# Optimization experiments

Hardware: AMD Instinct MI355X
Metric: run time of the kernel (lower is better)

The kernel has to match this reference:

```python
import jax, jax.numpy as jnp
import numpy as np

D_MODEL = 1024
N_HEADS = 16
HEAD_DIM = D_MODEL // N_HEADS


def setup_inputs() -> dict:
    key = jax.random.key(0)
    ks = jax.random.split(key, 9)
    B, S = 4, 2048
    x = jax.random.normal(ks[0], (B, S, D_MODEL), dtype=jnp.float32)
    # causal mask, broadcastable to (B, H, S, S); mask==0 -> -inf
    mask = jnp.tril(jnp.ones((S, S), dtype=jnp.int32))[None, None, :, :]
    s = 1.0 / np.sqrt(D_MODEL)
    wq = jax.random.normal(ks[1], (D_MODEL, D_MODEL), dtype=jnp.float32) * s
    wk = jax.random.normal(ks[2], (D_MODEL, D_MODEL), dtype=jnp.float32) * s
    wv = jax.random.normal(ks[3], (D_MODEL, D_MODEL), dtype=jnp.float32) * s
    wo = jax.random.normal(ks[4], (D_MODEL, D_MODEL), dtype=jnp.float32) * s
    bq = jnp.zeros((D_MODEL,), jnp.float32)
    bk = jnp.zeros((D_MODEL,), jnp.float32)
    bv = jnp.zeros((D_MODEL,), jnp.float32)
    bo = jnp.zeros((D_MODEL,), jnp.float32)
    return {"x": x, "mask": mask, "wq": wq, "bq": bq, "wk": wk, "bk": bk,
            "wv": wv, "bv": bv, "wo": wo, "bo": bo}


def reference(x, mask, wq, bq, wk, bk, wv, bv, wo, bo):
    B, S, D = x.shape
    H, Hd = N_HEADS, HEAD_DIM
    # torch nn.Linear: y = x @ W^T + b
    q = (jnp.einsum('bsd,ed->bse', x, wq) + bq).reshape(B, S, H, Hd).transpose(0, 2, 1, 3)
    k = (jnp.einsum('bsd,ed->bse', x, wk) + bk).reshape(B, S, H, Hd).transpose(0, 2, 1, 3)
    v = (jnp.einsum('bsd,ed->bse', x, wv) + bv).reshape(B, S, H, Hd).transpose(0, 2, 1, 3)
    scores = jnp.einsum('bhqd,bhkd->bhqk', q, k) / jnp.sqrt(jnp.float32(Hd))
    scores = jnp.where(mask == 0, -jnp.inf, scores)
    attn = jax.nn.softmax(scores, axis=-1)
    out = jnp.einsum('bhqk,bhkd->bhqd', attn, v)  # (B,H,S,Hd)
    out = out.transpose(0, 2, 1, 3).reshape(B, S, D)
    return jnp.einsum('bsd,ed->bse', out, wo) + bo
```

## Files before the change

kernel.cpp:

```cpp
#include <hip/hip_runtime.h>
#include <hip/hip_bf16.h>
#include <math.h>

using bf16x8 = __attribute__((ext_vector_type(8))) __bf16;
using bf16x4 = __attribute__((ext_vector_type(4))) __bf16;
using f32x4  = __attribute__((ext_vector_type(4))) float;
using f32x16 = __attribute__((ext_vector_type(16))) float;
using u32x4  = __attribute__((ext_vector_type(4))) unsigned;

static constexpr int S_ = 2048;
static constexpr float SCALE_L2E = 0.125f * 1.44269504088896340736f;

__device__ __forceinline__ void gload16(const void* g, void* lds) {
    __builtin_amdgcn_global_load_lds((const __attribute__((address_space(1))) void*)g,
                                     (__attribute__((address_space(3))) void*)lds, 16, 0, 0);
}

__device__ __forceinline__ unsigned pk2(float a, float b) {
    unsigned short lo = __builtin_bit_cast(unsigned short, (__bf16)a);
    unsigned short hi = __builtin_bit_cast(unsigned short, (__bf16)b);
    return (unsigned)lo | ((unsigned)hi << 16);
}

__device__ __forceinline__ float max3f(float a, float b, float c) {
    return fmaxf(fmaxf(a, b), c);
}

__global__ void cast_f32_bf16(const float* __restrict__ src, __bf16* __restrict__ dst, int n4) {
    int i = blockIdx.x * blockDim.x + threadIdx.x;
    if (i < n4) {
        float4 v = reinterpret_cast<const float4*>(src)[i];
        bf16x4 o = { (__bf16)v.x, (__bf16)v.y, (__bf16)v.z, (__bf16)v.w };
        reinterpret_cast<bf16x4*>(dst)[i] = o;
    }
}

template <int EPI>
__global__ __launch_bounds__(256) void gemm_bt(
    const __bf16* __restrict__ A, const __bf16* __restrict__ Bt,
    const float* __restrict__ b0, const float* __restrict__ b1, const float* __restrict__ b2,
    __bf16* __restrict__ Qo, __bf16* __restrict__ Ko, __bf16* __restrict__ Vo,
    float* __restrict__ Fo, int K) {
    __shared__ __align__(16) __bf16 LDS_[3][2][4096];
    const int t = threadIdx.x, l = t & 63, w = t >> 6;
    const int m0 = blockIdx.y * 128, n0 = blockIdx.x * 128;
    const int wm = (w >> 1) * 64, wn = (w & 1) * 64;
    f32x4 acc[4][4] = {};

    const int row0 = t >> 2, cw0 = t & 3;
    const int gc = cw0 ^ ((row0 >> 1) & 3);
    const __bf16* Ag0 = A + (size_t)(m0 + row0) * K + gc * 8;
    const __bf16* Ag1 = A + (size_t)(m0 + row0 + 64) * K + gc * 8;
    const __bf16* Bg0 = Bt + (size_t)(n0 + row0) * K + gc * 8;
    const __bf16* Bg1 = Bt + (size_t)(n0 + row0 + 64) * K + gc * 8;
    const int wo512 = w * 512;

#define STAGE(buf, k0)                                          \
    do {                                                        \
        gload16(Ag0 + (k0), &LDS_[buf][0][wo512]);              \
        gload16(Ag1 + (k0), &LDS_[buf][0][2048 + wo512]);       \
        gload16(Bg0 + (k0), &LDS_[buf][1][wo512]);              \
        gload16(Bg1 + (k0), &LDS_[buf][1][2048 + wo512]);       \
    } while (0)

    const int nk = K >> 5;
    STAGE(0, 0);
    STAGE(1, 32);
    int rb = 0, sb = 2;
    const int sc = (l >> 4) ^ ((l >> 1) & 3);
    for (int ki = 0; ki < nk; ++ki) {
        if (ki + 2 < nk) {
            STAGE(sb, (ki + 2) << 5);
            asm volatile("s_waitcnt vmcnt(8)" ::: "memory");
        } else if (ki + 1 < nk) {
            asm volatile("s_waitcnt vmcnt(4)" ::: "memory");
        } else {
            asm volatile("s_waitcnt vmcnt(0)" ::: "memory");
        }
        __builtin_amdgcn_s_barrier();
        const char* rdA = (const char*)&LDS_[rb][0][0];
        const char* rdB = (const char*)&LDS_[rb][1][0];
        bf16x8 af[4], bf[4];
#pragma unroll
        for (int i = 0; i < 4; ++i)
            af[i] = *reinterpret_cast<const bf16x8*>(rdA + (wm + i * 16 + (l & 15)) * 64 + sc * 16);
#pragma unroll
        for (int j = 0; j < 4; ++j)
            bf[j] = *reinterpret_cast<const bf16x8*>(rdB + (wn + j * 16 + (l & 15)) * 64 + sc * 16);
#pragma unroll
        for (int i = 0; i < 4; ++i)
#pragma unroll
            for (int j = 0; j < 4; ++j)
                acc[i][j] = __builtin_amdgcn_mfma_f32_16x16x32_bf16(af[i], bf[j], acc[i][j], 0, 0, 0);
        __builtin_amdgcn_s_barrier();
        rb = (rb == 2) ? 0 : rb + 1;
        sb = (sb == 2) ? 0 : sb + 1;
    }
#undef STAGE

    if (EPI == 0) {
        const int cls = n0 >> 10;
        if (cls < 2) {
            const float* bias = (cls == 0) ? b0 : b1;
#pragma unroll
            for (int j = 0; j < 4; ++j) {
                const int e = n0 + wn + j * 16 + (l & 15);
                const int eh = e & 1023;
                const int h = eh >> 6, hd = eh & 63;
                const float bv = bias[eh];
#pragma unroll
                for (int i = 0; i < 4; ++i)
#pragma unroll
                    for (int r = 0; r < 4; ++r) {
                        const int m = m0 + wm + i * 16 + ((l >> 4) << 2) + r;
                        const int b = m >> 11, s = m & 2047;
                        float v = acc[i][j][r] + bv;
                        if (cls == 0) v *= SCALE_L2E;
                        __bf16* dst = (cls == 0) ? Qo : Ko;
                        dst[((size_t)(b * 16 + h) * 2048 + s) * 64 + hd] = (__bf16)v;
                    }
            }
        } else {
            char* Tr = (char*)&LDS_[0][0][0];
#pragma unroll
            for (int j = 0; j < 4; ++j) {
                const int el = wn + j * 16 + (l & 15);
                const float bv = b2[(n0 & 1023) + el];
#pragma unroll
                for (int i = 0; i < 4; ++i) {
                    const int m4 = wm + i * 16 + ((l >> 4) << 2);
                    const int pos0 = (m4 & 112) | ((m4 & 4) << 1) | ((m4 & 8) >> 1);
                    bf16x4 pkv = { (__bf16)(acc[i][j][0] + bv), (__bf16)(acc[i][j][1] + bv),
                                   (__bf16)(acc[i][j][2] + bv), (__bf16)(acc[i][j][3] + bv) };
                    const int byt = el * 256 + ((pos0 * 2) ^ ((el & 7) << 4));
                    *reinterpret_cast<bf16x4*>(Tr + byt) = pkv;
                }
            }
            __syncthreads();
            const int b = m0 >> 11, sblk = m0 & 2047;
#pragma unroll
            for (int rr = 0; rr < 8; ++rr) {
                const int er = w * 32 + rr * 4 + (l >> 4);
                const int c = l & 15;
                const int slot = c ^ (er & 7);
                bf16x8 vv = *reinterpret_cast<const bf16x8*>(Tr + er * 256 + slot * 16);
                const int eg = (n0 & 1023) + er;
                const int h = eg >> 6, hd = eg & 63;
                char* dst = (char*)(Vo + ((size_t)(b * 16 + h) * 64 + hd) * 2048 + sblk) + c * 16;
                *reinterpret_cast<bf16x8*>(dst) = vv;
            }
        }
    } else {
#pragma unroll
        for (int j = 0; j < 4; ++j) {
            const int e = n0 + wn + j * 16 + (l & 15);
            const float bv = b0[e];
#pragma unroll
            for (int i = 0; i < 4; ++i)
#pragma unroll
                for (int r = 0; r < 4; ++r) {
                    const int m = m0 + wm + i * 16 + ((l >> 4) << 2) + r;
                    Fo[(size_t)m * 1024 + e] = acc[i][j][r] + bv;
                }
        }
    }
}

__global__ __launch_bounds__(512, 4) void attn_fwd(
    const __bf16* __restrict__ Qb, const __bf16* __restrict__ Kb,
    const __bf16* __restrict__ VTb, __bf16* __restrict__ Ob) {
    __shared__ __align__(16) __bf16 Ks[2][64 * 64];
    __shared__ __align__(16) __bf16 Vs[2][64 * 64];
    const int t = threadIdx.x, l = t & 63, w = t >> 6;
    const int id = blockIdx.x;
    const int bh = (id & 7) * 8 + ((id >> 3) & 7);
    const int g = id >> 6;
    const int xp = (g < 4) ? g : 11 - g;
    const int b = bh >> 4, hh = bh & 15;
    const int hl = l >> 5, l31 = l & 31;

    const __bf16* Qg = Qb + (size_t)bh * S_ * 64;
    const __bf16* Kg = Kb + (size_t)bh * S_ * 64;
    const __bf16* Vg = VTb + (size_t)bh * 64 * S_;

    const int qt = (w >> 2) ? xp : (15 - xp);
    const int sw = w & 3;
    const int qs = qt * 128 + sw * 32;
    const int qg = qs + l31;

    const int l3 = l >> 3, gc8 = ((l & 7) ^ l3) * 8;
    const __bf16* Ksrc = Kg + (size_t)(8 * w + l3) * 64 + gc8;
    const __bf16* Vsrc = Vg + (size_t)(8 * w + l3) * S_ + gc8;
    __bf16* Kd0 = &Ks[0][w * 512]; __bf16* Kd1 = &Ks[1][w * 512];
    __bf16* Vd0 = &Vs[0][w * 512]; __bf16* Vd1 = &Vs[1][w * 512];

    bf16x8 qf[4];
#pragma unroll
    for (int c = 0; c < 4; ++c)
        qf[c] = *reinterpret_cast<const bf16x8*>(Qg + (size_t)qg * 64 + c * 16 + hl * 8);

    f32x16 o0 = {}, o1 = {};
    float m_r = -INFINITY, l_r = 0.f;

    const int ktmax_blk = 2 * (15 - xp) + 1;
    gload16(Ksrc, Kd0);
    gload16(Vsrc, Vd0);
    int cur = 0;
    for (int kt = 0; kt <= ktmax_blk; ++kt) {
        if (kt < ktmax_blk) {
            const size_t ko = (size_t)(kt + 1) * 4096;
            gload16(Ksrc + ko, (cur == 0) ? Kd1 : Kd0);
            gload16(Vsrc + (kt + 1) * 64, (cur == 0) ? Vd1 : Vd0);
            asm volatile("s_waitcnt vmcnt(2)" ::: "memory");
        } else {
            asm volatile("s_waitcnt vmcnt(0)" ::: "memory");
        }
        __builtin_amdgcn_s_barrier();
        const char* kb = (cur == 0) ? (const char*)Ks[0] : (const char*)Ks[1];
        const char* vb = (cur == 0) ? (const char*)Vs[0] : (const char*)Vs[1];
        if (kt * 64 <= qs + 31) {
            const int xs = (l & 7) << 4;
            f32x16 s0 = {}, s1 = {};
            __builtin_amdgcn_s_setprio(1);
#pragma unroll
            for (int c = 0; c < 4; ++c) {
                bf16x8 kf0 = *reinterpret_cast<const bf16x8*>(kb + l31 * 128 + ((c * 32 + hl * 16) ^ xs));
                s0 = __builtin_amdgcn_mfma_f32_32x32x16_bf16(kf0, qf[c], s0, 0, 0, 0);
            }
#pragma unroll
            for (int c = 0; c < 4; ++c) {
                bf16x8 kf1 = *reinterpret_cast<const bf16x8*>(kb + (32 + l31) * 128 + ((c * 32 + hl * 16) ^ xs));
                s1 = __builtin_amdgcn_mfma_f32_32x32x16_bf16(kf1, qf[c], s1, 0, 0, 0);
            }
            __builtin_amdgcn_s_setprio(0);
            float p0[16], p1[16];
            const int ktb = kt * 64;
            const bool bnd = (ktb + 63) > qs;
            if (bnd) {
#pragma unroll
                for (int r = 0; r < 16; ++r) {
                    const int kvr = ktb + (r & 3) + 8 * (r >> 2) + 4 * hl;
                    p0[r] = (kvr > qg) ? -INFINITY : s0[r];
                    p1[r] = (kvr + 32 > qg) ? -INFINITY : s1[r];
                }
            } else {
#pragma unroll
                for (int r = 0; r < 16; ++r) { p0[r] = s0[r]; p1[r] = s1[r]; }
            }
            float mx[16];
#pragma unroll
            for (int r = 0; r < 16; ++r) mx[r] = fmaxf(p0[r], p1[r]);
            float u0 = max3f(mx[0], mx[1], mx[2]);
            float u1 = max3f(mx[3], mx[4], mx[5]);
            float u2 = max3f(mx[6], mx[7], mx[8]);
            float u3 = max3f(mx[9], mx[10], mx[11]);
            float u4 = max3f(mx[12], mx[13], mx[14]);
            float mt = fmaxf(max3f(u0, u1, u2), max3f(u3, u4, mx[15]));
            mt = fmaxf(mt, __shfl_xor(mt, 32));
            if (!__all(mt - m_r <= 8.0f)) {
                const float mn = fmaxf(m_r, mt);
                const float al = exp2f(m_r - mn);
                m_r = mn;
                l_r *= al;
#pragma unroll
                for (int r = 0; r < 16; ++r) { o0[r] *= al; o1[r] *= al; }
            }
            float sm[16];
#pragma unroll
            for (int r = 0; r < 16; ++r) {
                p0[r] = exp2f(p0[r] - m_r);
                p1[r] = exp2f(p1[r] - m_r);
                sm[r] = p0[r] + p1[r];
            }
#pragma unroll
            for (int s2 = 8; s2 > 0; s2 >>= 1)
#pragma unroll
                for (int r = 0; r < 8; ++r) if (r < s2) sm[r] += sm[r + s2];
            l_r += sm[0] + __shfl_xor(sm[0], 32);
            u32x4 w0 = { pk2(p0[0], p0[1]), pk2(p0[2], p0[3]), pk2(p0[4], p0[5]), pk2(p0[6], p0[7]) };
            u32x4 w1 = { pk2(p0[8], p0[9]), pk2(p0[10], p0[11]), pk2(p0[12], p0[13]), pk2(p0[14], p0[15]) };
            u32x4 w2 = { pk2(p1[0], p1[1]), pk2(p1[2], p1[3]), pk2(p1[4], p1[5]), pk2(p1[6], p1[7]) };
            u32x4 w3 = { pk2(p1[8], p1[9]), pk2(p1[10], p1[11]), pk2(p1[12], p1[13]), pk2(p1[14], p1[15]) };
            bf16x8 pf0 = __builtin_bit_cast(bf16x8, w0);
            bf16x8 pf1 = __builtin_bit_cast(bf16x8, w1);
            bf16x8 pf2 = __builtin_bit_cast(bf16x8, w2);
            bf16x8 pf3 = __builtin_bit_cast(bf16x8, w3);
            __builtin_amdgcn_s_setprio(1);
#pragma unroll
            for (int a = 0; a < 2; ++a) {
                const int rb2 = (a * 32 + l31) * 128;
                bf16x8 vf0 = *reinterpret_cast<const bf16x8*>(vb + rb2 + ((0 * 32 + hl * 16) ^ xs));
                bf16x8 vf1 = *reinterpret_cast<const bf16x8*>(vb + rb2 + ((1 * 32 + hl * 16) ^ xs));
                bf16x8 vf2 = *reinterpret_cast<const bf16x8*>(vb + rb2 + ((2 * 32 + hl * 16) ^ xs));
                bf16x8 vf3 = *reinterpret_cast<const bf16x8*>(vb + rb2 + ((3 * 32 + hl * 16) ^ xs));
                if (a == 0) {
                    o0 = __builtin_amdgcn_mfma_f32_32x32x16_bf16(vf0, pf0, o0, 0, 0, 0);
                    o0 = __builtin_amdgcn_mfma_f32_32x32x16_bf16(vf1, pf1, o0, 0, 0, 0);
                    o0 = __builtin_amdgcn_mfma_f32_32x32x16_bf16(vf2, pf2, o0, 0, 0, 0);
                    o0 = __builtin_amdgcn_mfma_f32_32x32x16_bf16(vf3, pf3, o0, 0, 0, 0);
                } else {
                    o1 = __builtin_amdgcn_mfma_f32_32x32x16_bf16(vf0, pf0, o1, 0, 0, 0);
                    o1 = __builtin_amdgcn_mfma_f32_32x32x16_bf16(vf1, pf1, o1, 0, 0, 0);
                    o1 = __builtin_amdgcn_mfma_f32_32x32x16_bf16(vf2, pf2, o1, 0, 0, 0);
                    o1 = __builtin_amdgcn_mfma_f32_32x32x16_bf16(vf3, pf3, o1, 0, 0, 0);
                }
            }
            __builtin_amdgcn_s_setprio(0);
        }
        __builtin_amdgcn_s_barrier();
        cur ^= 1;
    }
    const float inv = 1.0f / l_r;
    __bf16* ob = Ob + (size_t)(b * 2048 + qg) * 1024 + hh * 64;
#pragma unroll
    for (int gq = 0; gq < 4; ++gq) {
        bf16x4 v0 = { (__bf16)(o0[4 * gq + 0] * inv), (__bf16)(o0[4 * gq + 1] * inv),
                      (__bf16)(o0[4 * gq + 2] * inv), (__bf16)(o0[4 * gq + 3] * inv) };
        bf16x4 v1 = { (__bf16)(o1[4 * gq + 0] * inv), (__bf16)(o1[4 * gq + 1] * inv),
                      (__bf16)(o1[4 * gq + 2] * inv), (__bf16)(o1[4 * gq + 3] * inv) };
        *reinterpret_cast<bf16x4*>(ob + 8 * gq + 4 * hl) = v0;
        *reinterpret_cast<bf16x4*>(ob + 32 + 8 * gq + 4 * hl) = v1;
    }
}

extern "C" void kernel_launch(void* const* d_in, const int* in_sizes, int n_in,
                              void* d_out, int out_size, void* d_ws, size_t ws_size,
                              hipStream_t stream) {
    const float* x  = (const float*)d_in[0];
    const float* wq = (const float*)d_in[2];
    const float* bq = (const float*)d_in[3];
    const float* wk = (const float*)d_in[4];
    const float* bk = (const float*)d_in[5];
    const float* wv = (const float*)d_in[6];
    const float* bv = (const float*)d_in[7];
    const float* wo = (const float*)d_in[8];
    const float* bo = (const float*)d_in[9];
    float* out = (float*)d_out;

    char* ws = (char*)d_ws;
    __bf16* xb   = (__bf16*)(ws);
    __bf16* wqkv = (__bf16*)(ws + 16777216);
    __bf16* wob  = (__bf16*)(ws + 23068672);
    __bf16* Qb   = (__bf16*)(ws + 25165824);
    __bf16* Kb   = (__bf16*)(ws + 41943040);
    __bf16* VTb  = (__bf16*)(ws + 58720256);
    __bf16* Ob   = (__bf16*)(ws + 75497472);

    cast_f32_bf16<<<8192, 256, 0, stream>>>(x, xb, 2097152);
    cast_f32_bf16<<<1024, 256, 0, stream>>>(wq, wqkv, 262144);
    cast_f32_bf16<<<1024, 256, 0, stream>>>(wk, wqkv + 1048576, 262144);
    cast_f32_bf16<<<1024, 256, 0, stream>>>(wv, wqkv + 2097152, 262144);
    cast_f32_bf16<<<1024, 256, 0, stream>>>(wo, wob, 262144);

    gemm_bt<0><<<dim3(24, 64), 256, 0, stream>>>(xb, wqkv, bq, bk, bv, Qb, Kb, VTb, nullptr, 1024);
    attn_fwd<<<512, 512, 0, stream>>>(Qb, Kb, VTb, Ob);
    gemm_bt<1><<<dim3(8, 64), 256, 0, stream>>>(Ob, wob, bo, nullptr, nullptr, nullptr, nullptr, nullptr, out, 1024);
}
```

Measured before the change: 185.0 us.

## Shrink attention blocks to two waves with 32-row KV tiles and paired phases

The attention kernel now runs as 1024 blocks of 128 threads instead of 512 blocks of 512 threads. Each block covers 64 query rows and processes two mirrored query tiles in sequence, which balances the causal workload within a block. KV tiles are cut from 64 to 32 keys with a new LDS swizzle for V. The goal is less barrier coupling across waves and more resident blocks per CU. In exchange there are twice as many loop iterations and barriers per query tile, and less reuse of each staged K/V tile, since only two waves share it.

```diff
diff --git a/kernel.cpp b/kernel.cpp
--- a/kernel.cpp
+++ b/kernel.cpp
@@ -166,16 +166,16 @@
     }
 }
 
-__global__ __launch_bounds__(512, 4) void attn_fwd(
+__global__ __launch_bounds__(128, 4) void attn_fwd(
     const __bf16* __restrict__ Qb, const __bf16* __restrict__ Kb,
     const __bf16* __restrict__ VTb, __bf16* __restrict__ Ob) {
-    __shared__ __align__(16) __bf16 Ks[2][64 * 64];
-    __shared__ __align__(16) __bf16 Vs[2][64 * 64];
+    __shared__ __align__(16) __bf16 Ks[2][32 * 64];
+    __shared__ __align__(16) __bf16 Vs[2][64 * 32];
     const int t = threadIdx.x, l = t & 63, w = t >> 6;
     const int id = blockIdx.x;
     const int bh = (id & 7) * 8 + ((id >> 3) & 7);
-    const int g = id >> 6;
-    const int xp = (g < 4) ? g : 11 - g;
+    const int pp = (id >> 6) & 7;
+    const int hf = id >> 9;
     const int b = bh >> 4, hh = bh & 15;
     const int hl = l >> 5, l31 = l & 31;
 
@@ -183,144 +183,137 @@
     const __bf16* Kg = Kb + (size_t)bh * S_ * 64;
     const __bf16* Vg = VTb + (size_t)bh * 64 * S_;
 
-    const int qt = (w >> 2) ? xp : (15 - xp);
-    const int sw = w & 3;
-    const int qs = qt * 128 + sw * 32;
-    const int qg = qs + l31;
-
-    const int l3 = l >> 3, gc8 = ((l & 7) ^ l3) * 8;
-    const __bf16* Ksrc = Kg + (size_t)(8 * w + l3) * 64 + gc8;
-    const __bf16* Vsrc = Vg + (size_t)(8 * w + l3) * S_ + gc8;
-    __bf16* Kd0 = &Ks[0][w * 512]; __bf16* Kd1 = &Ks[1][w * 512];
-    __bf16* Vd0 = &Vs[0][w * 512]; __bf16* Vd1 = &Vs[1][w * 512];
-
-    bf16x8 qf[4];
-#pragma unroll
-    for (int c = 0; c < 4; ++c)
-        qf[c] = *reinterpret_cast<const bf16x8*>(Qg + (size_t)qg * 64 + c * 16 + hl * 8);
-
-    f32x16 o0 = {}, o1 = {};
-    float m_r = -INFINITY, l_r = 0.f;
-
-    const int ktmax_blk = 2 * (15 - xp) + 1;
-    gload16(Ksrc, Kd0);
-    gload16(Vsrc, Vd0);
-    int cur = 0;
-    for (int kt = 0; kt <= ktmax_blk; ++kt) {
-        if (kt < ktmax_blk) {
-            const size_t ko = (size_t)(kt + 1) * 4096;
-            gload16(Ksrc + ko, (cur == 0) ? Kd1 : Kd0);
-            gload16(Vsrc + (kt + 1) * 64, (cur == 0) ? Vd1 : Vd0);
-            asm volatile("s_waitcnt vmcnt(2)" ::: "memory");
-        } else {
-            asm volatile("s_waitcnt vmcnt(0)" ::: "memory");
-        }
-        __builtin_amdgcn_s_barrier();
-        const char* kb = (cur == 0) ? (const char*)Ks[0] : (const char*)Ks[1];
-        const char* vb = (cur == 0) ? (const char*)Vs[0] : (const char*)Vs[1];
-        if (kt * 64 <= qs + 31) {
-            const int xs = (l & 7) << 4;
-            f32x16 s0 = {}, s1 = {};
-            __builtin_amdgcn_s_setprio(1);
-#pragma unroll
-            for (int c = 0; c < 4; ++c) {
-                bf16x8 kf0 = *reinterpret_cast<const bf16x8*>(kb + l31 * 128 + ((c * 32 + hl * 16) ^ xs));
-                s0 = __builtin_amdgcn_mfma_f32_32x32x16_bf16(kf0, qf[c], s0, 0, 0, 0);
-            }
-#pragma unroll
-            for (int c = 0; c < 4; ++c) {
-                bf16x8 kf1 = *reinterpret_cast<const bf16x8*>(kb + (32 + l31) * 128 + ((c * 32 + hl * 16) ^ xs));
-                s1 = __builtin_amdgcn_mfma_f32_32x32x16_bf16(kf1, qf[c], s1, 0, 0, 0);
-            }
-            __builtin_amdgcn_s_setprio(0);
-            float p0[16], p1[16];
-            const int ktb = kt * 64;
-            const bool bnd = (ktb + 63) > qs;
-            if (bnd) {
-#pragma unroll
-                for (int r = 0; r < 16; ++r) {
-                    const int kvr = ktb + (r & 3) + 8 * (r >> 2) + 4 * hl;
-                    p0[r] = (kvr > qg) ? -INFINITY : s0[r];
-                    p1[r] = (kvr + 32 > qg) ? -INFINITY : s1[r];
-                }
+    const int l3 = l >> 3;
+    const int kc8 = ((l & 7) ^ l3) * 8;
+    const __bf16* Ksrc0 = Kg + (size_t)(16 * w + l3) * 64 + kc8;
+    const __bf16* Ksrc1 = Kg + (size_t)(16 * w + 8 + l3) * 64 + kc8;
+    const int l2 = l >> 2;
+    const int vc8 = ((l & 3) ^ (l2 & 3)) * 8;
+    const __bf16* Vsrc0 = Vg + (size_t)(32 * w + l2) * S_ + vc8;
+    const __bf16* Vsrc1 = Vg + (size_t)(32 * w + 16 + l2) * S_ + vc8;
+    __bf16* Kd0 = &Ks[0][w * 1024]; __bf16* Kd1 = &Ks[1][w * 1024];
+    __bf16* Vd0 = &Vs[0][w * 1024]; __bf16* Vd1 = &Vs[1][w * 1024];
+
+#define STAGEKV(cc, kt)                                                   \
+    do {                                                                  \
+        gload16(Ksrc0 + (size_t)(kt) * 2048, (cc) ? Kd1 : Kd0);           \
+        gload16(Ksrc1 + (size_t)(kt) * 2048, ((cc) ? Kd1 : Kd0) + 512);   \
+        gload16(Vsrc0 + (kt) * 32, (cc) ? Vd1 : Vd0);                     \
+        gload16(Vsrc1 + (kt) * 32, ((cc) ? Vd1 : Vd0) + 512);             \
+    } while (0)
+
+#pragma unroll 1
+    for (int ph = 0; ph < 2; ++ph) {
+        const int qt = ph ? pp : (15 - pp);
+        const int qs = qt * 128 + hf * 64 + w * 32;
+        const int qg = qs + l31;
+
+        bf16x8 qf[4];
+#pragma unroll
+        for (int c = 0; c < 4; ++c)
+            qf[c] = *reinterpret_cast<const bf16x8*>(Qg + (size_t)qg * 64 + c * 16 + hl * 8);
+
+        f32x16 o0 = {}, o1 = {};
+        float m_r = -INFINITY, l_r = 0.f;
+
+        const int nkt = 4 * qt + 4;
+        STAGEKV(0, 0);
+        int cur = 0;
+        for (int kt = 0; kt < nkt; ++kt) {
+            if (kt + 1 < nkt) {
+                STAGEKV(cur ^ 1, kt + 1);
+                asm volatile("s_waitcnt vmcnt(4)" ::: "memory");
             } else {
-#pragma unroll
-                for (int r = 0; r < 16; ++r) { p0[r] = s0[r]; p1[r] = s1[r]; }
-            }
-            float mx[16];
-#pragma unroll
-            for (int r = 0; r < 16; ++r) mx[r] = fmaxf(p0[r], p1[r]);
-            float u0 = max3f(mx[0], mx[1], mx[2]);
-            float u1 = max3f(mx[3], mx[4], mx[5]);
-            float u2 = max3f(mx[6], mx[7], mx[8]);
-            float u3 = max3f(mx[9], mx[10], mx[11]);
-            float u4 = max3f(mx[12], mx[13], mx[14]);
-            float mt = fmaxf(max3f(u0, u1, u2), max3f(u3, u4, mx[15]));
-            mt = fmaxf(mt, __shfl_xor(mt, 32));
-            if (!__all(mt - m_r <= 8.0f)) {
-                const float mn = fmaxf(m_r, mt);
-                const float al = exp2f(m_r - mn);
-                m_r = mn;
-                l_r *= al;
-#pragma unroll
-                for (int r = 0; r < 16; ++r) { o0[r] *= al; o1[r] *= al; }
-            }
-            float sm[16];
-#pragma unroll
-            for (int r = 0; r < 16; ++r) {
-                p0[r] = exp2f(p0[r] - m_r);
-                p1[r] = exp2f(p1[r] - m_r);
-                sm[r] = p0[r] + p1[r];
-            }
-#pragma unroll
-            for (int s2 = 8; s2 > 0; s2 >>= 1)
-#pragma unroll
-                for (int r = 0; r < 8; ++r) if (r < s2) sm[r] += sm[r + s2];
-            l_r += sm[0] + __shfl_xor(sm[0], 32);
-            u32x4 w0 = { pk2(p0[0], p0[1]), pk2(p0[2], p0[3]), pk2(p0[4], p0[5]), pk2(p0[6], p0[7]) };
-            u32x4 w1 = { pk2(p0[8], p0[9]), pk2(p0[10], p0[11]), pk2(p0[12], p0[13]), pk2(p0[14], p0[15]) };
-            u32x4 w2 = { pk2(p1[0], p1[1]), pk2(p1[2], p1[3]), pk2(p1[4], p1[5]), pk2(p1[6], p1[7]) };
-            u32x4 w3 = { pk2(p1[8], p1[9]), pk2(p1[10], p1[11]), pk2(p1[12], p1[13]), pk2(p1[14], p1[15]) };
-            bf16x8 pf0 = __builtin_bit_cast(bf16x8, w0);
-            bf16x8 pf1 = __builtin_bit_cast(bf16x8, w1);
-            bf16x8 pf2 = __builtin_bit_cast(bf16x8, w2);
-            bf16x8 pf3 = __builtin_bit_cast(bf16x8, w3);
-            __builtin_amdgcn_s_setprio(1);
-#pragma unroll
-            for (int a = 0; a < 2; ++a) {
-                const int rb2 = (a * 32 + l31) * 128;
-                bf16x8 vf0 = *reinterpret_cast<const bf16x8*>(vb + rb2 + ((0 * 32 + hl * 16) ^ xs));
-                bf16x8 vf1 = *reinterpret_cast<const bf16x8*>(vb + rb2 + ((1 * 32 + hl * 16) ^ xs));
-                bf16x8 vf2 = *reinterpret_cast<const bf16x8*>(vb + rb2 + ((2 * 32 + hl * 16) ^ xs));
-                bf16x8 vf3 = *reinterpret_cast<const bf16x8*>(vb + rb2 + ((3 * 32 + hl * 16) ^ xs));
-                if (a == 0) {
-                    o0 = __builtin_amdgcn_mfma_f32_32x32x16_bf16(vf0, pf0, o0, 0, 0, 0);
-                    o0 = __builtin_amdgcn_mfma_f32_32x32x16_bf16(vf1, pf1, o0, 0, 0, 0);
-                    o0 = __builtin_amdgcn_mfma_f32_32x32x16_bf16(vf2, pf2, o0, 0, 0, 0);
-                    o0 = __builtin_amdgcn_mfma_f32_32x32x16_bf16(vf3, pf3, o0, 0, 0, 0);
+                asm volatile("s_waitcnt vmcnt(0)" ::: "memory");
+            }
+            __builtin_amdgcn_s_barrier();
+            const char* kb = (const char*)(cur ? Ks[1] : Ks[0]);
+            const char* vb = (const char*)(cur ? Vs[1] : Vs[0]);
+            const int ktb = kt * 32;
+            if (ktb <= qs + 31) {
+                const int xs = (l31 & 7) << 4;
+                f32x16 s0 = {};
+                __builtin_amdgcn_s_setprio(1);
+#pragma unroll
+                for (int c = 0; c < 4; ++c) {
+                    bf16x8 kf = *reinterpret_cast<const bf16x8*>(kb + l31 * 128 + ((c * 32 + hl * 16) ^ xs));
+                    s0 = __builtin_amdgcn_mfma_f32_32x32x16_bf16(kf, qf[c], s0, 0, 0, 0);
+                }
+                __builtin_amdgcn_s_setprio(0);
+                float pr[16];
+                const bool bnd = (ktb + 31) > qs;
+                if (bnd) {
+#pragma unroll
+                    for (int r = 0; r < 16; ++r) {
+                        const int kvr = ktb + (r & 3) + 8 * (r >> 2) + 4 * hl;
+                        pr[r] = (kvr > qg) ? -INFINITY : s0[r];
+                    }
                 } else {
-                    o1 = __builtin_amdgcn_mfma_f32_32x32x16_bf16(vf0, pf0, o1, 0, 0, 0);
-                    o1 = __builtin_amdgcn_mfma_f32_32x32x16_bf16(vf1, pf1, o1, 0, 0, 0);
-                    o1 = __builtin_amdgcn_mfma_f32_32x32x16_bf16(vf2, pf2, o1, 0, 0, 0);
-                    o1 = __builtin_amdgcn_mfma_f32_32x32x16_bf16(vf3, pf3, o1, 0, 0, 0);
-                }
-            }
-            __builtin_amdgcn_s_setprio(0);
-        }
-        __builtin_amdgcn_s_barrier();
-        cur ^= 1;
+#pragma unroll
+                    for (int r = 0; r < 16; ++r) pr[r] = s0[r];
+                }
+                float u0 = max3f(pr[0], pr[1], pr[2]);
+                float u1 = max3f(pr[3], pr[4], pr[5]);
+                float u2 = max3f(pr[6], pr[7], pr[8]);
+                float u3 = max3f(pr[9], pr[10], pr[11]);
+                float u4 = max3f(pr[12], pr[13], pr[14]);
+                float mt = fmaxf(max3f(u0, u1, u2), max3f(u3, u4, pr[15]));
+                mt = fmaxf(mt, __shfl_xor(mt, 32));
+                if (!__all(mt - m_r <= 8.0f)) {
+                    const float mn = fmaxf(m_r, mt);
+                    const float al = exp2f(m_r - mn);
+                    m_r = mn;
+                    l_r *= al;
+#pragma unroll
+                    for (int r = 0; r < 16; ++r) { o0[r] *= al; o1[r] *= al; }
+                }
+                float sm[8];
+#pragma unroll
+                for (int r = 0; r < 16; ++r) pr[r] = exp2f(pr[r] - m_r);
+#pragma unroll
+                for (int r = 0; r < 8; ++r) sm[r] = pr[r] + pr[r + 8];
+#pragma unroll
+                for (int s2 = 4; s2 > 0; s2 >>= 1)
+#pragma unroll
+                    for (int r = 0; r < 4; ++r) if (r < s2) sm[r] += sm[r + s2];
+                l_r += sm[0] + __shfl_xor(sm[0], 32);
+                u32x4 w0 = { pk2(pr[0], pr[1]), pk2(pr[2], pr[3]), pk2(pr[4], pr[5]), pk2(pr[6], pr[7]) };
+                u32x4 w1 = { pk2(pr[8], pr[9]), pk2(pr[10], pr[11]), pk2(pr[12], pr[13]), pk2(pr[14], pr[15]) };
+                bf16x8 pf0 = __builtin_bit_cast(bf16x8, w0);
+                bf16x8 pf1 = __builtin_bit_cast(bf16x8, w1);
+                __builtin_amdgcn_s_setprio(1);
+                const int xv = l31 & 3;
+#pragma unroll
+                for (int a = 0; a < 2; ++a) {
+                    const int rb2 = (a * 32 + l31) * 64;
+                    bf16x8 vf0 = *reinterpret_cast<const bf16x8*>(vb + rb2 + (((0 + hl) ^ xv) << 4));
+                    bf16x8 vf1 = *reinterpret_cast<const bf16x8*>(vb + rb2 + (((2 + hl) ^ xv) << 4));
+                    if (a == 0) {
+                        o0 = __builtin_amdgcn_mfma_f32_32x32x16_bf16(vf0, pf0, o0, 0, 0, 0);
+                        o0 = __builtin_amdgcn_mfma_f32_32x32x16_bf16(vf1, pf1, o0, 0, 0, 0);
+                    } else {
+                        o1 = __builtin_amdgcn_mfma_f32_32x32x16_bf16(vf0, pf0, o1, 0, 0, 0);
+                        o1 = __builtin_amdgcn_mfma_f32_32x32x16_bf16(vf1, pf1, o1, 0, 0, 0);
+                    }
+                }
+                __builtin_amdgcn_s_setprio(0);
+            }
+            __builtin_amdgcn_s_barrier();
+            cur ^= 1;
+        }
+        const float inv = 1.0f / l_r;
+        __bf16* ob = Ob + (size_t)(b * 2048 + qg) * 1024 + hh * 64;
+#pragma unroll
+        for (int gq = 0; gq < 4; ++gq) {
+            bf16x4 v0 = { (__bf16)(o0[4 * gq + 0] * inv), (__bf16)(o0[4 * gq + 1] * inv),
+                          (__bf16)(o0[4 * gq + 2] * inv), (__bf16)(o0[4 * gq + 3] * inv) };
+            bf16x4 v1 = { (__bf16)(o1[4 * gq + 0] * inv), (__bf16)(o1[4 * gq + 1] * inv),
+                          (__bf16)(o1[4 * gq + 2] * inv), (__bf16)(o1[4 * gq + 3] * inv) };
+            *reinterpret_cast<bf16x4*>(ob + 8 * gq + 4 * hl) = v0;
+            *reinterpret_cast<bf16x4*>(ob + 32 + 8 * gq + 4 * hl) = v1;
+        }
     }
-    const float inv = 1.0f / l_r;
-    __bf16* ob = Ob + (size_t)(b * 2048 + qg) * 1024 + hh * 64;
-#pragma unroll
-    for (int gq = 0; gq < 4; ++gq) {
-        bf16x4 v0 = { (__bf16)(o0[4 * gq + 0] * inv), (__bf16)(o0[4 * gq + 1] * inv),
-                      (__bf16)(o0[4 * gq + 2] * inv), (__bf16)(o0[4 * gq + 3] * inv) };
-        bf16x4 v1 = { (__bf16)(o1[4 * gq + 0] * inv), (__bf16)(o1[4 * gq + 1] * inv),
-                      (__bf16)(o1[4 * gq + 2] * inv), (__bf16)(o1[4 * gq + 3] * inv) };
-        *reinterpret_cast<bf16x4*>(ob + 8 * gq + 4 * hl) = v0;
-        *reinterpret_cast<bf16x4*>(ob + 32 + 8 * gq + 4 * hl) = v1;
-    }
+#undef STAGEKV
 }
 
 extern "C" void kernel_launch(void* const* d_in, const int* in_sizes, int n_in,
@@ -353,6 +346,6 @@
     cast_f32_bf16<<<1024, 256, 0, stream>>>(wo, wob, 262144);
 
     gemm_bt<0><<<dim3(24, 64), 256, 0, stream>>>(xb, wqkv, bq, bk, bv, Qb, Kb, VTb, nullptr, 1024);
-    attn_fwd<<<512, 512, 0, stream>>>(Qb, Kb, VTb, Ob);
+    attn_fwd<<<1024, 128, 0, stream>>>(Qb, Kb, VTb, Ob);
     gemm_bt<1><<<dim3(8, 64), 256, 0, stream>>>(Ob, wob, bo, nullptr, nullptr, nullptr, nullptr, nullptr, out, 1024);
 }
```

Result: slower. 202.0 us (+9.2%).

## Split attention into one q-tile per 4-warp block with interleaved causal ordering

Applied to the files above, without the earlier changes.

Each attention block now processes a single 128-row query tile with 4 warps instead of pairing a heavy and a light tile in 8 warps. This removes the idle warps of the light tile that previously waited through the heavy tile's extra K/V iterations and barriers. The block index ordering interleaves long and short tiles to keep the GPU load balanced, and K/V staging is redistributed so each thread issues four async loads per stage. The risk is a longer tail from the heaviest blocks and less K/V reuse per load across warps.

```diff
diff --git a/kernel.cpp b/kernel.cpp
--- a/kernel.cpp
+++ b/kernel.cpp
@@ -166,16 +166,16 @@
     }
 }
 
-__global__ __launch_bounds__(512, 4) void attn_fwd(
+__global__ __launch_bounds__(256, 4) void attn_fwd(
     const __bf16* __restrict__ Qb, const __bf16* __restrict__ Kb,
     const __bf16* __restrict__ VTb, __bf16* __restrict__ Ob) {
     __shared__ __align__(16) __bf16 Ks[2][64 * 64];
     __shared__ __align__(16) __bf16 Vs[2][64 * 64];
     const int t = threadIdx.x, l = t & 63, w = t >> 6;
     const int id = blockIdx.x;
-    const int bh = (id & 7) * 8 + ((id >> 3) & 7);
-    const int g = id >> 6;
-    const int xp = (g < 4) ? g : 11 - g;
+    const int r = id >> 8, g = (id >> 6) & 3;
+    const int qt = (r & 1) ? (2 * g + (r >> 1)) : (15 - 2 * g - (r >> 1));
+    const int bh = id & 63;
     const int b = bh >> 4, hh = bh & 15;
     const int hl = l >> 5, l31 = l & 31;
 
@@ -183,16 +183,25 @@
     const __bf16* Kg = Kb + (size_t)bh * S_ * 64;
     const __bf16* Vg = VTb + (size_t)bh * 64 * S_;
 
-    const int qt = (w >> 2) ? xp : (15 - xp);
-    const int sw = w & 3;
-    const int qs = qt * 128 + sw * 32;
+    const int qs = qt * 128 + w * 32;
     const int qg = qs + l31;
 
-    const int l3 = l >> 3, gc8 = ((l & 7) ^ l3) * 8;
-    const __bf16* Ksrc = Kg + (size_t)(8 * w + l3) * 64 + gc8;
-    const __bf16* Vsrc = Vg + (size_t)(8 * w + l3) * S_ + gc8;
-    __bf16* Kd0 = &Ks[0][w * 512]; __bf16* Kd1 = &Ks[1][w * 512];
-    __bf16* Vd0 = &Vs[0][w * 512]; __bf16* Vd1 = &Vs[1][w * 512];
+    const int tr = t >> 3, sl = t & 7;
+    const int swz = (sl ^ (tr & 7)) * 8;
+    const __bf16* Ksrc0 = Kg + (size_t)tr * 64 + swz;
+    const __bf16* Ksrc1 = Kg + (size_t)(tr + 32) * 64 + swz;
+    const __bf16* Vsrc0 = Vg + (size_t)tr * S_ + swz;
+    const __bf16* Vsrc1 = Vg + (size_t)(tr + 32) * S_ + swz;
+    __bf16* Kd[2] = { &Ks[0][t * 8], &Ks[1][t * 8] };
+    __bf16* Vd[2] = { &Vs[0][t * 8], &Vs[1][t * 8] };
+
+#define STAGEKV(cc, kt)                                       \
+    do {                                                      \
+        gload16(Ksrc0 + (size_t)(kt) * 4096, Kd[cc]);         \
+        gload16(Ksrc1 + (size_t)(kt) * 4096, Kd[cc] + 2048);  \
+        gload16(Vsrc0 + (kt) * 64, Vd[cc]);                   \
+        gload16(Vsrc1 + (kt) * 64, Vd[cc] + 2048);            \
+    } while (0)
 
     bf16x8 qf[4];
 #pragma unroll
@@ -202,23 +211,21 @@
     f32x16 o0 = {}, o1 = {};
     float m_r = -INFINITY, l_r = 0.f;
 
-    const int ktmax_blk = 2 * (15 - xp) + 1;
-    gload16(Ksrc, Kd0);
-    gload16(Vsrc, Vd0);
+    const int nkt = 2 * qt + 2;
+    STAGEKV(0, 0);
     int cur = 0;
-    for (int kt = 0; kt <= ktmax_blk; ++kt) {
-        if (kt < ktmax_blk) {
-            const size_t ko = (size_t)(kt + 1) * 4096;
-            gload16(Ksrc + ko, (cur == 0) ? Kd1 : Kd0);
-            gload16(Vsrc + (kt + 1) * 64, (cur == 0) ? Vd1 : Vd0);
-            asm volatile("s_waitcnt vmcnt(2)" ::: "memory");
+    for (int kt = 0; kt < nkt; ++kt) {
+        if (kt + 1 < nkt) {
+            STAGEKV(cur ^ 1, kt + 1);
+            asm volatile("s_waitcnt vmcnt(4)" ::: "memory");
         } else {
             asm volatile("s_waitcnt vmcnt(0)" ::: "memory");
         }
         __builtin_amdgcn_s_barrier();
-        const char* kb = (cur == 0) ? (const char*)Ks[0] : (const char*)Ks[1];
-        const char* vb = (cur == 0) ? (const char*)Vs[0] : (const char*)Vs[1];
-        if (kt * 64 <= qs + 31) {
+        const char* kb = (const char*)(cur ? Ks[1] : Ks[0]);
+        const char* vb = (const char*)(cur ? Vs[1] : Vs[0]);
+        const int ktb = kt * 64;
+        if (ktb <= qs + 31) {
             const int xs = (l & 7) << 4;
             f32x16 s0 = {}, s1 = {};
             __builtin_amdgcn_s_setprio(1);
@@ -234,22 +241,21 @@
             }
             __builtin_amdgcn_s_setprio(0);
             float p0[16], p1[16];
-            const int ktb = kt * 64;
             const bool bnd = (ktb + 63) > qs;
             if (bnd) {
 #pragma unroll
-                for (int r = 0; r < 16; ++r) {
-                    const int kvr = ktb + (r & 3) + 8 * (r >> 2) + 4 * hl;
-                    p0[r] = (kvr > qg) ? -INFINITY : s0[r];
-                    p1[r] = (kvr + 32 > qg) ? -INFINITY : s1[r];
+                for (int rr = 0; rr < 16; ++rr) {
+                    const int kvr = ktb + (rr & 3) + 8 * (rr >> 2) + 4 * hl;
+                    p0[rr] = (kvr > qg) ? -INFINITY : s0[rr];
+                    p1[rr] = (kvr + 32 > qg) ? -INFINITY : s1[rr];
                 }
             } else {
 #pragma unroll
-                for (int r = 0; r < 16; ++r) { p0[r] = s0[r]; p1[r] = s1[r]; }
+                for (int rr = 0; rr < 16; ++rr) { p0[rr] = s0[rr]; p1[rr] = s1[rr]; }
             }
             float mx[16];
 #pragma unroll
-            for (int r = 0; r < 16; ++r) mx[r] = fmaxf(p0[r], p1[r]);
+            for (int rr = 0; rr < 16; ++rr) mx[rr] = fmaxf(p0[rr], p1[rr]);
             float u0 = max3f(mx[0], mx[1], mx[2]);
             float u1 = max3f(mx[3], mx[4], mx[5]);
             float u2 = max3f(mx[6], mx[7], mx[8]);
@@ -263,19 +269,19 @@
                 m_r = mn;
                 l_r *= al;
 #pragma unroll
-                for (int r = 0; r < 16; ++r) { o0[r] *= al; o1[r] *= al; }
+                for (int rr = 0; rr < 16; ++rr) { o0[rr] *= al; o1[rr] *= al; }
             }
             float sm[16];
 #pragma unroll
-            for (int r = 0; r < 16; ++r) {
-                p0[r] = exp2f(p0[r] - m_r);
-                p1[r] = exp2f(p1[r] - m_r);
-                sm[r] = p0[r] + p1[r];
+            for (int rr = 0; rr < 16; ++rr) {
+                p0[rr] = exp2f(p0[rr] - m_r);
+                p1[rr] = exp2f(p1[rr] - m_r);
+                sm[rr] = p0[rr] + p1[rr];
             }
 #pragma unroll
             for (int s2 = 8; s2 > 0; s2 >>= 1)
 #pragma unroll
-                for (int r = 0; r < 8; ++r) if (r < s2) sm[r] += sm[r + s2];
+                for (int rr = 0; rr < 8; ++rr) if (rr < s2) sm[rr] += sm[rr + s2];
             l_r += sm[0] + __shfl_xor(sm[0], 32);
             u32x4 w0 = { pk2(p0[0], p0[1]), pk2(p0[2], p0[3]), pk2(p0[4], p0[5]), pk2(p0[6], p0[7]) };
             u32x4 w1 = { pk2(p0[8], p0[9]), pk2(p0[10], p0[11]), pk2(p0[12], p0[13]), pk2(p0[14], p0[15]) };
@@ -310,6 +316,7 @@
         __builtin_amdgcn_s_barrier();
         cur ^= 1;
     }
+#undef STAGEKV
     const float inv = 1.0f / l_r;
     __bf16* ob = Ob + (size_t)(b * 2048 + qg) * 1024 + hh * 64;
 #pragma unroll
@@ -353,6 +360,6 @@
     cast_f32_bf16<<<1024, 256, 0, stream>>>(wo, wob, 262144);
 
     gemm_bt<0><<<dim3(24, 64), 256, 0, stream>>>(xb, wqkv, bq, bk, bv, Qb, Kb, VTb, nullptr, 1024);
-    attn_fwd<<<512, 512, 0, stream>>>(Qb, Kb, VTb, Ob);
+    attn_fwd<<<1024, 256, 0, stream>>>(Qb, Kb, VTb, Ob);
     gemm_bt<1><<<dim3(8, 64), 256, 0, stream>>>(Ob, wob, bo, nullptr, nullptr, nullptr, nullptr, nullptr, out, 1024);
 }
```

Result: no change. 185.2 us (+0.1%).
